# Kernel optimization log

Hardware: AMD Instinct MI355X
Metric: run time of the kernel (lower is better)

Reference implementation:

```python
import jax, jax.numpy as jnp
import numpy as np


def _hemisphere(radius=1.0, n=5):
    # replicates DiffuseShader.generate_hemisphere with sample=(5j,5j)
    u, v = np.mgrid[0:np.pi:n * 1j, 0:np.pi:n * 1j]
    x = (radius * np.cos(u) * np.sin(v)).flatten()
    y = (radius * np.sin(u) * np.sin(v)).flatten()
    z = (radius * np.cos(v)).flatten()
    return jnp.asarray(np.c_[x, y, z], dtype=jnp.float32)


def _diffuse_forward(V, COL, OPA, p, l, normals, hemi_vecs, indices, pointindex):
    P, S, N = p.shape[0], hemi_vecs.shape[0], V.shape[0]
    local = pointindex % P
    # --- project_hemisphere_projection: Rodrigues rotation local->global ---
    u = l[None, :] - p                                      # [P,3]
    u_hat = u / jnp.linalg.norm(u, axis=1, keepdims=True)
    v_loc = jnp.broadcast_to(jnp.array([0.0, -1.0, 0.0], p.dtype), u_hat.shape)
    c = -u_hat[:, 1:2]                                      # rowwise dot(v_loc, u_hat), [P,1]
    w = jnp.cross(v_loc, u_hat)                             # [P,3]
    z0 = jnp.zeros_like(w[:, 0])
    vmat = jnp.stack([jnp.stack([z0, -w[:, 2], w[:, 1]], -1),
                      jnp.stack([w[:, 2], z0, -w[:, 0]], -1),
                      jnp.stack([-w[:, 1], w[:, 0], z0], -1)], axis=1)  # [P,3,3] skew(w)
    R = jnp.eye(3, dtype=p.dtype)[None] + vmat + jnp.matmul(vmat, vmat) / (1.0 + c)[..., None]
    lh = jnp.einsum('pij,sj->psi', R, hemi_vecs) + l        # [P,S,3]
    o = jnp.broadcast_to(p[:, None, :], (P, S, 3))
    d = lh - o
    # --- get_intersection: ray/plane distances ---
    nrm = jnp.cross(V[:, 1] - V[:, 0], V[:, 2] - V[:, 0])
    nrm = nrm / jnp.linalg.norm(nrm, axis=1, keepdims=True)  # [N,3]
    kk = -jnp.sum(nrm * V[:, 3], axis=1)                     # [N]
    vo = o.reshape(P * S, 3) @ nrm.T                         # [P*S,N]
    vd = d.reshape(P * S, 3) @ nrm.T
    t = (-(kk[None, :] + vo) / vd).reshape(P, N, S)          # faithful to torch .view(P,N,S) on the [P*S,N] buffer
    surf = indices[pointindex, 0]
    mat = indices[pointindex, 1]
    empty = jnp.zeros((P, N, S), bool).at[local, surf, :].set(True)
    viable = (t > -1e-4) & (t < 1.0) & (~empty)
    # --- barycentric condition test ---
    r = o[:, None, :, :] + t[..., None] * d[:, None, :, :]   # [P,N,S,3]
    a0 = V[:, 0, 0][None, :, None]; a1 = V[:, 0, 1][None, :, None]; a2 = V[:, 0, 2][None, :, None]
    b0 = V[:, 1, 0][None, :, None]; b1 = V[:, 1, 1][None, :, None]; b2 = V[:, 1, 2][None, :, None]
    c0 = V[:, 2, 0][None, :, None]; c1 = V[:, 2, 1][None, :, None]; c2 = V[:, 2, 2][None, :, None]
    r0, r1, r2 = r[..., 0], r[..., 1], r[..., 2]
    A = a0 * r2 - a2 * r0
    B = a0 * b2 - a2 * b0
    C = a0 * r1 - a1 * r0
    D = a0 * b1 - a1 * b0
    E = a0 * c2 - a2 * c0
    F = B * (a1 * c0 - a0 * c1)
    gam = (D * (A * D - B * C)) / (D * (E * D + F))
    beta = (C + gam * (a1 * c0 - a0 * c1)) / D
    alpha = (r0 - (beta * b0 + gam * c0)) / a0
    mask = jnp.where(viable & (beta > 0.0) & (gam > 0.0) & (alpha > 0.0), 1.0, 0.0).astype(jnp.float32)
    col = COL[surf, mat]                                     # [P,3]
    opa = jnp.clip(OPA[surf, mat], 0.0, 1.0)                 # [P]
    reflected_ray = l[None, :] - p                           # [P,3]
    return mask, col, opa, reflected_ray


def setup_inputs() -> dict:
    P, N, M, G = 512, 1024, 8, 2048
    key = jax.random.key(0)
    ks = jax.random.split(key, 8)
    V = jax.random.normal(ks[0], (N, 4, 3), jnp.float32)
    indices = jax.random.randint(ks[1], (G, 2), 0, M)
    pointindex = jax.random.randint(ks[2], (P,), 0, G)
    COL = jax.random.uniform(ks[3], (N, M, 3), jnp.float32)
    OPA = jax.random.uniform(ks[4], (N, M), jnp.float32)
    p = jax.random.normal(ks[5], (P, 3), jnp.float32) * 5.0
    l = jax.random.normal(ks[6], (3,), jnp.float32) * 10.0 + 20.0
    normals = jax.random.normal(ks[7], (N, 3), jnp.float32)
    return {"V": V, "indices": indices, "pointindex": pointindex, "COL": COL,
            "OPA": OPA, "p": p, "l": l, "normals": normals, "it": 0,
            "hemi_vecs": _hemisphere(1.0, 5)}


def reference(V, indices, pointindex, COL, OPA, p, l, normals, it, hemi_vecs):
    return _diffuse_forward(V, COL, OPA, p, l, normals, hemi_vecs, indices, pointindex)
```

## Files before the change

### kernel.cpp

```cpp
#include <hip/hip_runtime.h>
#include <math.h>

#define NP   512
#define NT   1024
#define NS   25
#define NPS  (NP*NS)
#define MASKN (NP*NT*NS)

#define DSA_OFF  0
#define PD_OFF   51200
#define NX_OFF   53248
#define NY_OFF   54272
#define NZ_OFF   55296
#define KK_OFF   56320
#define W_OFF    57344
#define EMPTY_OFF ((size_t)67584 * 8)

__global__ void prep_points(const float* __restrict__ p,
                            const float* __restrict__ l,
                            const float* __restrict__ hemi,
                            double* __restrict__ ws) {
    int idx = blockIdx.x * 256 + threadIdx.x;
    if (idx >= NPS) return;
    int pi = idx / NS, si = idx % NS;
    double px = p[pi*3+0], py = p[pi*3+1], pz = p[pi*3+2];
    double lx = l[0], ly = l[1], lz = l[2];
    double ux = lx - px, uy = ly - py, uz = lz - pz;
    double nrm = sqrt(ux*ux + uy*uy + uz*uz);
    ux /= nrm; uy /= nrm; uz /= nrm;
    double c = -uy;
    double wx = -uz, wz = ux;
    double m01 = -wz, m02 = 0.0;
    double m10 =  wz, m12 = -wx;
    double m21 =  wx, m20 = 0.0;
    double q00 = m01*m10;
    double q01 = 0.0, q10 = 0.0;
    double q02 = m01*m12;
    double q11 = m10*m01 + m12*m21;
    double q12 = 0.0, q21 = 0.0;
    double q20 = m21*m10;
    double q22 = m21*m12;
    double ic = 1.0 + c;
    double r00 = 1.0 + q00/ic, r01 = m01 + q01/ic, r02 = m02 + q02/ic;
    double r10 = m10 + q10/ic, r11 = 1.0 + q11/ic, r12 = m12 + q12/ic;
    double r20 = m20 + q20/ic, r21 = m21 + q21/ic, r22 = 1.0 + q22/ic;
    double hx = hemi[si*3+0], hy = hemi[si*3+1], hz = hemi[si*3+2];
    double lhx = r00*hx + r01*hy + r02*hz + lx;
    double lhy = r10*hx + r11*hy + r12*hz + ly;
    double lhz = r20*hx + r21*hy + r22*hz + lz;
    double* dsA = ws + DSA_OFF;
    dsA[idx*4+0] = lhx - px;
    dsA[idx*4+1] = lhy - py;
    dsA[idx*4+2] = lhz - pz;
    dsA[idx*4+3] = 0.0;
}

__device__ __forceinline__ double sgn(double x) {
    return (x > 0.0) ? 1.0 : ((x < 0.0) ? -1.0 : 0.0);
}

__global__ void prep_tris(const float* __restrict__ V,
                          double* __restrict__ ws,
                          unsigned* __restrict__ emptyMask) {
    int n = blockIdx.x * 256 + threadIdx.x;
    if (n < NP) emptyMask[n] = 0u;
    if (n >= NT) return;
    const float* v = V + n*12;
    double a0=v[0], a1=v[1], a2=v[2];
    double b0=v[3], b1=v[4], b2=v[5];
    double c0=v[6], c1=v[7], c2=v[8];
    double v3x=v[9], v3y=v[10], v3z=v[11];
    double e1x=b0-a0, e1y=b1-a1, e1z=b2-a2;
    double e2x=c0-a0, e2y=c1-a1, e2z=c2-a2;
    double cx = e1y*e2z - e1z*e2y;
    double cy = e1z*e2x - e1x*e2z;
    double cz = e1x*e2y - e1y*e2x;
    double nn = sqrt(cx*cx + cy*cy + cz*cz);
    double nx = cx/nn, ny = cy/nn, nz = cz/nn;
    double kk = -(nx*v3x + ny*v3y + nz*v3z);
    double Bv = a0*b2 - a2*b0;
    double Dv = a0*b1 - a1*b0;
    double Ec = a0*c2 - a2*c0;
    double G2 = a1*c0 - a0*c1;
    double Fc = Bv*G2;
    double gd = Dv*(Ec*Dv + Fc);
    double gq = Dv*gd;
    double dq = Dv*c0;
    double aq = a0*gq;
    double WGr0 = a1*Bv - a2*Dv, WGr1 = -(a0*Bv), WGr2 = a0*Dv;
    double dg = Dv*G2;
    double WBr0 = -(a1*gd) + dg*WGr0;
    double WBr1 =  a0*gd  + dg*WGr1;
    double WBr2 =            dg*WGr2;
    double dd = Dv*dq;
    double WAr0 = gq - b0*WBr0 - dd*WGr0;
    double WAr1 =    - b0*WBr1 - dd*WGr1;
    double WAr2 =    - b0*WBr2 - dd*WGr2;
    double sg = sgn(Dv*gd), sb = sgn(gq), sa = sgn(aq);
    ws[NX_OFF + n] = nx;
    ws[NY_OFF + n] = ny;
    ws[NZ_OFF + n] = nz;
    ws[KK_OFF + n] = kk;
    double* W = ws + W_OFF + n*10;
    W[0] = WGr0*sg; W[1] = WGr1*sg; W[2] = WGr2*sg;
    W[3] = WBr0*sb; W[4] = WBr1*sb; W[5] = WBr2*sb;
    W[6] = WAr0*sa; W[7] = WAr1*sa; W[8] = WAr2*sa;
    W[9] = 0.0;
}

__global__ void prep_scatter(const int* __restrict__ indices,
                             const int* __restrict__ pointindex,
                             const float* __restrict__ COL,
                             const float* __restrict__ OPA,
                             const float* __restrict__ p,
                             const float* __restrict__ l,
                             unsigned* __restrict__ emptyMask,
                             float* __restrict__ out,
                             double* __restrict__ ws) {
    int i = blockIdx.x * 256 + threadIdx.x;
    if (i >= NP) return;
    int pidx = pointindex[i];
    int local = pidx & (NP - 1);
    int surf = indices[pidx*2 + 0];
    int mat  = indices[pidx*2 + 1];
    atomicOr(&emptyMask[local], 1u << surf);
    float* colOut = out + MASKN;
    float* opaOut = out + MASKN + 3*NP;
    float* refOut = out + MASKN + 4*NP;
    colOut[i*3+0] = COL[(surf*8+mat)*3+0];
    colOut[i*3+1] = COL[(surf*8+mat)*3+1];
    colOut[i*3+2] = COL[(surf*8+mat)*3+2];
    float o = OPA[surf*8+mat];
    opaOut[i] = fminf(fmaxf(o, 0.0f), 1.0f);
    refOut[i*3+0] = (float)((double)l[0] - (double)p[i*3+0]);
    refOut[i*3+1] = (float)((double)l[1] - (double)p[i*3+1]);
    refOut[i*3+2] = (float)((double)l[2] - (double)p[i*3+2]);
    double* pd = ws + PD_OFF;
    pd[i*4+0] = (double)p[i*3+0];
    pd[i*4+1] = (double)p[i*3+1];
    pd[i*4+2] = (double)p[i*3+2];
    pd[i*4+3] = 0.0;
}

__global__ __launch_bounds__(256) void diffuse_main(
        const double* __restrict__ ws,
        const unsigned* __restrict__ emptyMask,
        float* __restrict__ out) {
    __shared__ double sW[42][10];
    __shared__ double sdx[25], sdy[25], sdz[25];

    const unsigned ps = blockIdx.x;
    const unsigned pp = ps / 25u;
    const unsigned q  = ps - pp * 25u;
    const unsigned nn0 = (q << 10) / 25u;
    const unsigned tid = threadIdx.x;

    const double* Wg = ws + W_OFF;
    {
        unsigned i = tid;
        if (i < 210u) {
            unsigned row = i / 5u, col = i - row * 5u;
            unsigned gn = nn0 + row; if (gn > 1023u) gn = 1023u;
            const double2 v = *(const double2*)(Wg + gn*10u + col*2u);
            sW[row][col*2u]   = v.x;
            sW[row][col*2u+1] = v.y;
        }
        if (i < 25u) {
            const double* dr = ws + DSA_OFF + (pp*25u + i)*4u;
            sdx[i] = dr[0]; sdy[i] = dr[1]; sdz[i] = dr[2];
        }
    }
    const double sx = ws[DSA_OFF + ps*4u + 0];
    const double sy = ws[DSA_OFF + ps*4u + 1];
    const double sz = ws[DSA_OFF + ps*4u + 2];
    const double ox = ws[PD_OFF + pp*4u + 0];
    const double oy = ws[PD_OFF + pp*4u + 1];
    const double oz = ws[PD_OFF + pp*4u + 2];
    const unsigned em = emptyMask[pp];
    __syncthreads();

    const unsigned n0 = tid * 4u;
    const double2 nxa = *(const double2*)(ws + NX_OFF + n0);
    const double2 nxb = *(const double2*)(ws + NX_OFF + n0 + 2);
    const double2 nya = *(const double2*)(ws + NY_OFF + n0);
    const double2 nyb = *(const double2*)(ws + NY_OFF + n0 + 2);
    const double2 nza = *(const double2*)(ws + NZ_OFF + n0);
    const double2 nzb = *(const double2*)(ws + NZ_OFF + n0 + 2);
    const double2 kka = *(const double2*)(ws + KK_OFF + n0);
    const double2 kkb = *(const double2*)(ws + KK_OFF + n0 + 2);
    const unsigned rem0 = (q << 10) + n0;

    float res[4];
    #pragma unroll
    for (int k = 0; k < 4; ++k) {
        const double nxv = (k < 2) ? (k ? nxa.y : nxa.x) : (k == 3 ? nxb.y : nxb.x);
        const double nyv = (k < 2) ? (k ? nya.y : nya.x) : (k == 3 ? nyb.y : nyb.x);
        const double nzv = (k < 2) ? (k ? nza.y : nza.x) : (k == 3 ? nzb.y : nzb.x);
        const double kkv = (k < 2) ? (k ? kka.y : kka.x) : (k == 3 ? kkb.y : kkb.x);

        const double vd = fma(sz, nzv, fma(sy, nyv, sx * nxv));
        const double tt = fma(oz, nzv, fma(oy, nyv, fma(ox, nxv, kkv)));
        const double e1 = fma(1e-4, vd, -tt);
        const double e2 = vd + tt;

        const unsigned rem = rem0 + (unsigned)k;
        const unsigned nn = rem / 25u;
        const unsigned ss = rem - nn * 25u;
        const bool empty = (nn < 8u) && ((em >> nn) & 1u);

        const double dxv = sdx[ss], dyv = sdy[ss], dzv = sdz[ss];
        const double R0 = fma(-tt, dxv, vd * ox);
        const double R1 = fma(-tt, dyv, vd * oy);
        const double R2 = fma(-tt, dzv, vd * oz);

        const double* w = sW[nn - nn0];
        const double dG = fma(R2, w[2], fma(R1, w[1], R0 * w[0]));
        const double dB = fma(R2, w[5], fma(R1, w[4], R0 * w[3]));
        const double dA = fma(R2, w[8], fma(R1, w[7], R0 * w[6]));

        const bool ok = (e1 * vd > 0.0) && (e2 * vd > 0.0) && !empty
                     && (dG * vd > 0.0) && (dB * vd > 0.0) && (dA * vd > 0.0);
        res[k] = ok ? 1.0f : 0.0f;
    }
    *(float4*)(out + ps*1024u + n0) = make_float4(res[0], res[1], res[2], res[3]);
}

extern "C" void kernel_launch(void* const* d_in, const int* in_sizes, int n_in,
                              void* d_out, int out_size, void* d_ws, size_t ws_size,
                              hipStream_t stream) {
    const float* V         = (const float*)d_in[0];
    const int*   indices   = (const int*)  d_in[1];
    const int*   pointindex= (const int*)  d_in[2];
    const float* COL       = (const float*)d_in[3];
    const float* OPA       = (const float*)d_in[4];
    const float* p         = (const float*)d_in[5];
    const float* l         = (const float*)d_in[6];
    const float* hemi      = (const float*)d_in[9];

    float* out = (float*)d_out;
    double* ws = (double*)d_ws;
    unsigned* emptyMask = (unsigned*)((char*)d_ws + EMPTY_OFF);

    prep_points<<<(NPS + 255)/256, 256, 0, stream>>>(p, l, hemi, ws);
    prep_tris<<<(NT + 255)/256, 256, 0, stream>>>(V, ws, emptyMask);
    prep_scatter<<<(NP + 255)/256, 256, 0, stream>>>(indices, pointindex, COL, OPA,
                                                     p, l, emptyMask, out, ws);
    diffuse_main<<<NPS, 256, 0, stream>>>(ws, emptyMask, out);
}
```

Baseline: 41.13 us.

## Fuse prep kernels into one launch and simplify main-kernel sign tests

Merges the three preprocessing kernels into one launch that splits work by block range, removing two kernel launches and their serialization gaps. In the main kernel, the per-element divide by 25 becomes an incremental counter, the six multiply-and-compare sign tests become one XOR/OR on the high words of the doubles, and the empty-surface check is compiled in only for blocks with q==0. The shared weight row is padded from 10 to 11 doubles. The sign-bit trick treats zero and negative-zero differently from the old strict > 0 compare, which can change results in edge cases.

```diff
diff --git a/kernel.cpp b/kernel.cpp
--- a/kernel.cpp
+++ b/kernel.cpp
@@ -16,137 +16,187 @@
 #define W_OFF    57344
 #define EMPTY_OFF ((size_t)67584 * 8)
 
-__global__ void prep_points(const float* __restrict__ p,
-                            const float* __restrict__ l,
-                            const float* __restrict__ hemi,
-                            double* __restrict__ ws) {
-    int idx = blockIdx.x * 256 + threadIdx.x;
-    if (idx >= NPS) return;
-    int pi = idx / NS, si = idx % NS;
-    double px = p[pi*3+0], py = p[pi*3+1], pz = p[pi*3+2];
-    double lx = l[0], ly = l[1], lz = l[2];
-    double ux = lx - px, uy = ly - py, uz = lz - pz;
-    double nrm = sqrt(ux*ux + uy*uy + uz*uz);
-    ux /= nrm; uy /= nrm; uz /= nrm;
-    double c = -uy;
-    double wx = -uz, wz = ux;
-    double m01 = -wz, m02 = 0.0;
-    double m10 =  wz, m12 = -wx;
-    double m21 =  wx, m20 = 0.0;
-    double q00 = m01*m10;
-    double q01 = 0.0, q10 = 0.0;
-    double q02 = m01*m12;
-    double q11 = m10*m01 + m12*m21;
-    double q12 = 0.0, q21 = 0.0;
-    double q20 = m21*m10;
-    double q22 = m21*m12;
-    double ic = 1.0 + c;
-    double r00 = 1.0 + q00/ic, r01 = m01 + q01/ic, r02 = m02 + q02/ic;
-    double r10 = m10 + q10/ic, r11 = 1.0 + q11/ic, r12 = m12 + q12/ic;
-    double r20 = m20 + q20/ic, r21 = m21 + q21/ic, r22 = 1.0 + q22/ic;
-    double hx = hemi[si*3+0], hy = hemi[si*3+1], hz = hemi[si*3+2];
-    double lhx = r00*hx + r01*hy + r02*hz + lx;
-    double lhy = r10*hx + r11*hy + r12*hz + ly;
-    double lhz = r20*hx + r21*hy + r22*hz + lz;
-    double* dsA = ws + DSA_OFF;
-    dsA[idx*4+0] = lhx - px;
-    dsA[idx*4+1] = lhy - py;
-    dsA[idx*4+2] = lhz - pz;
-    dsA[idx*4+3] = 0.0;
-}
-
 __device__ __forceinline__ double sgn(double x) {
     return (x > 0.0) ? 1.0 : ((x < 0.0) ? -1.0 : 0.0);
 }
 
-__global__ void prep_tris(const float* __restrict__ V,
-                          double* __restrict__ ws,
-                          unsigned* __restrict__ emptyMask) {
-    int n = blockIdx.x * 256 + threadIdx.x;
-    if (n < NP) emptyMask[n] = 0u;
-    if (n >= NT) return;
-    const float* v = V + n*12;
-    double a0=v[0], a1=v[1], a2=v[2];
-    double b0=v[3], b1=v[4], b2=v[5];
-    double c0=v[6], c1=v[7], c2=v[8];
-    double v3x=v[9], v3y=v[10], v3z=v[11];
-    double e1x=b0-a0, e1y=b1-a1, e1z=b2-a2;
-    double e2x=c0-a0, e2y=c1-a1, e2z=c2-a2;
-    double cx = e1y*e2z - e1z*e2y;
-    double cy = e1z*e2x - e1x*e2z;
-    double cz = e1x*e2y - e1y*e2x;
-    double nn = sqrt(cx*cx + cy*cy + cz*cz);
-    double nx = cx/nn, ny = cy/nn, nz = cz/nn;
-    double kk = -(nx*v3x + ny*v3y + nz*v3z);
-    double Bv = a0*b2 - a2*b0;
-    double Dv = a0*b1 - a1*b0;
-    double Ec = a0*c2 - a2*c0;
-    double G2 = a1*c0 - a0*c1;
-    double Fc = Bv*G2;
-    double gd = Dv*(Ec*Dv + Fc);
-    double gq = Dv*gd;
-    double dq = Dv*c0;
-    double aq = a0*gq;
-    double WGr0 = a1*Bv - a2*Dv, WGr1 = -(a0*Bv), WGr2 = a0*Dv;
-    double dg = Dv*G2;
-    double WBr0 = -(a1*gd) + dg*WGr0;
-    double WBr1 =  a0*gd  + dg*WGr1;
-    double WBr2 =            dg*WGr2;
-    double dd = Dv*dq;
-    double WAr0 = gq - b0*WBr0 - dd*WGr0;
-    double WAr1 =    - b0*WBr1 - dd*WGr1;
-    double WAr2 =    - b0*WBr2 - dd*WGr2;
-    double sg = sgn(Dv*gd), sb = sgn(gq), sa = sgn(aq);
-    ws[NX_OFF + n] = nx;
-    ws[NY_OFF + n] = ny;
-    ws[NZ_OFF + n] = nz;
-    ws[KK_OFF + n] = kk;
-    double* W = ws + W_OFF + n*10;
-    W[0] = WGr0*sg; W[1] = WGr1*sg; W[2] = WGr2*sg;
-    W[3] = WBr0*sb; W[4] = WBr1*sb; W[5] = WBr2*sb;
-    W[6] = WAr0*sa; W[7] = WAr1*sa; W[8] = WAr2*sa;
-    W[9] = 0.0;
-}
-
-__global__ void prep_scatter(const int* __restrict__ indices,
-                             const int* __restrict__ pointindex,
-                             const float* __restrict__ COL,
-                             const float* __restrict__ OPA,
-                             const float* __restrict__ p,
-                             const float* __restrict__ l,
-                             unsigned* __restrict__ emptyMask,
-                             float* __restrict__ out,
-                             double* __restrict__ ws) {
-    int i = blockIdx.x * 256 + threadIdx.x;
-    if (i >= NP) return;
-    int pidx = pointindex[i];
-    int local = pidx & (NP - 1);
-    int surf = indices[pidx*2 + 0];
-    int mat  = indices[pidx*2 + 1];
-    atomicOr(&emptyMask[local], 1u << surf);
-    float* colOut = out + MASKN;
-    float* opaOut = out + MASKN + 3*NP;
-    float* refOut = out + MASKN + 4*NP;
-    colOut[i*3+0] = COL[(surf*8+mat)*3+0];
-    colOut[i*3+1] = COL[(surf*8+mat)*3+1];
-    colOut[i*3+2] = COL[(surf*8+mat)*3+2];
-    float o = OPA[surf*8+mat];
-    opaOut[i] = fminf(fmaxf(o, 0.0f), 1.0f);
-    refOut[i*3+0] = (float)((double)l[0] - (double)p[i*3+0]);
-    refOut[i*3+1] = (float)((double)l[1] - (double)p[i*3+1]);
-    refOut[i*3+2] = (float)((double)l[2] - (double)p[i*3+2]);
-    double* pd = ws + PD_OFF;
-    pd[i*4+0] = (double)p[i*3+0];
-    pd[i*4+1] = (double)p[i*3+1];
-    pd[i*4+2] = (double)p[i*3+2];
-    pd[i*4+3] = 0.0;
+__global__ void prep_all(const float* __restrict__ p,
+                         const float* __restrict__ l,
+                         const float* __restrict__ hemi,
+                         const float* __restrict__ V,
+                         const int* __restrict__ indices,
+                         const int* __restrict__ pointindex,
+                         const float* __restrict__ COL,
+                         const float* __restrict__ OPA,
+                         double* __restrict__ ws,
+                         unsigned* __restrict__ emptyMask,
+                         float* __restrict__ out) {
+    const int b = blockIdx.x, t = threadIdx.x;
+    if (b < 50) {
+        int idx = b * 256 + t;
+        int pi = idx / NS, si = idx % NS;
+        double px = p[pi*3+0], py = p[pi*3+1], pz = p[pi*3+2];
+        double lx = l[0], ly = l[1], lz = l[2];
+        double ux = lx - px, uy = ly - py, uz = lz - pz;
+        double nrm = sqrt(ux*ux + uy*uy + uz*uz);
+        ux /= nrm; uy /= nrm; uz /= nrm;
+        double c = -uy;
+        double wx = -uz, wz = ux;
+        double m01 = -wz, m10 = wz, m12 = -wx, m21 = wx;
+        double q00 = m01*m10;
+        double q02 = m01*m12;
+        double q11 = m10*m01 + m12*m21;
+        double q20 = m21*m10;
+        double q22 = m21*m12;
+        double ic = 1.0 + c;
+        double r00 = 1.0 + q00/ic, r01 = m01,            r02 = q02/ic;
+        double r10 = m10,          r11 = 1.0 + q11/ic,   r12 = m12;
+        double r20 = q20/ic,       r21 = m21,            r22 = 1.0 + q22/ic;
+        double hx = hemi[si*3+0], hy = hemi[si*3+1], hz = hemi[si*3+2];
+        double lhx = r00*hx + r01*hy + r02*hz + lx;
+        double lhy = r10*hx + r11*hy + r12*hz + ly;
+        double lhz = r20*hx + r21*hy + r22*hz + lz;
+        double* dsA = ws + DSA_OFF;
+        dsA[idx*4+0] = lhx - px;
+        dsA[idx*4+1] = lhy - py;
+        dsA[idx*4+2] = lhz - pz;
+        dsA[idx*4+3] = 0.0;
+    } else if (b < 54) {
+        int n = (b - 50) * 256 + t;
+        const float* v = V + n*12;
+        double a0=v[0], a1=v[1], a2=v[2];
+        double b0=v[3], b1=v[4], b2=v[5];
+        double c0=v[6], c1=v[7], c2=v[8];
+        double v3x=v[9], v3y=v[10], v3z=v[11];
+        double e1x=b0-a0, e1y=b1-a1, e1z=b2-a2;
+        double e2x=c0-a0, e2y=c1-a1, e2z=c2-a2;
+        double cx = e1y*e2z - e1z*e2y;
+        double cy = e1z*e2x - e1x*e2z;
+        double cz = e1x*e2y - e1y*e2x;
+        double nn = sqrt(cx*cx + cy*cy + cz*cz);
+        double nx = cx/nn, ny = cy/nn, nz = cz/nn;
+        double kk = -(nx*v3x + ny*v3y + nz*v3z);
+        double Bv = a0*b2 - a2*b0;
+        double Dv = a0*b1 - a1*b0;
+        double Ec = a0*c2 - a2*c0;
+        double G2 = a1*c0 - a0*c1;
+        double Fc = Bv*G2;
+        double gd = Dv*(Ec*Dv + Fc);
+        double gq = Dv*gd;
+        double dq = Dv*c0;
+        double aq = a0*gq;
+        double WGr0 = a1*Bv - a2*Dv, WGr1 = -(a0*Bv), WGr2 = a0*Dv;
+        double dg = Dv*G2;
+        double WBr0 = -(a1*gd) + dg*WGr0;
+        double WBr1 =  a0*gd  + dg*WGr1;
+        double WBr2 =            dg*WGr2;
+        double dd = Dv*dq;
+        double WAr0 = gq - b0*WBr0 - dd*WGr0;
+        double WAr1 =    - b0*WBr1 - dd*WGr1;
+        double WAr2 =    - b0*WBr2 - dd*WGr2;
+        double sg = sgn(Dv*gd), sb = sgn(gq), sa = sgn(aq);
+        ws[NX_OFF + n] = nx;
+        ws[NY_OFF + n] = ny;
+        ws[NZ_OFF + n] = nz;
+        ws[KK_OFF + n] = kk;
+        double* W = ws + W_OFF + n*10;
+        W[0] = WGr0*sg; W[1] = WGr1*sg; W[2] = WGr2*sg;
+        W[3] = WBr0*sb; W[4] = WBr1*sb; W[5] = WBr2*sb;
+        W[6] = WAr0*sa; W[7] = WAr1*sa; W[8] = WAr2*sa;
+        W[9] = 0.0;
+    } else {
+        emptyMask[t] = 0u;
+        emptyMask[t + 256] = 0u;
+        __syncthreads();
+        for (int i = t; i < NP; i += 256) {
+            int pidx = pointindex[i];
+            int local = pidx & (NP - 1);
+            int surf = indices[pidx*2 + 0];
+            int mat  = indices[pidx*2 + 1];
+            atomicOr(&emptyMask[local], 1u << surf);
+            float* colOut = out + MASKN;
+            float* opaOut = out + MASKN + 3*NP;
+            float* refOut = out + MASKN + 4*NP;
+            colOut[i*3+0] = COL[(surf*8+mat)*3+0];
+            colOut[i*3+1] = COL[(surf*8+mat)*3+1];
+            colOut[i*3+2] = COL[(surf*8+mat)*3+2];
+            float o = OPA[surf*8+mat];
+            opaOut[i] = fminf(fmaxf(o, 0.0f), 1.0f);
+            refOut[i*3+0] = (float)((double)l[0] - (double)p[i*3+0]);
+            refOut[i*3+1] = (float)((double)l[1] - (double)p[i*3+1]);
+            refOut[i*3+2] = (float)((double)l[2] - (double)p[i*3+2]);
+            double* pd = ws + PD_OFF;
+            pd[i*4+0] = (double)p[i*3+0];
+            pd[i*4+1] = (double)p[i*3+1];
+            pd[i*4+2] = (double)p[i*3+2];
+            pd[i*4+3] = 0.0;
+        }
+    }
+}
+
+template<bool HE>
+__device__ __forceinline__ void line_body(
+        const double* __restrict__ ws, const double (*sW)[11],
+        const double* sdx, const double* sdy, const double* sdz,
+        double sx, double sy, double sz, double ox, double oy, double oz,
+        unsigned em, unsigned nn0, unsigned q, unsigned ps, unsigned tid,
+        float* __restrict__ out) {
+    const unsigned n0 = tid * 4u;
+    const double2 nxa = *(const double2*)(ws + NX_OFF + n0);
+    const double2 nxb = *(const double2*)(ws + NX_OFF + n0 + 2);
+    const double2 nya = *(const double2*)(ws + NY_OFF + n0);
+    const double2 nyb = *(const double2*)(ws + NY_OFF + n0 + 2);
+    const double2 nza = *(const double2*)(ws + NZ_OFF + n0);
+    const double2 nzb = *(const double2*)(ws + NZ_OFF + n0 + 2);
+    const double2 kka = *(const double2*)(ws + KK_OFF + n0);
+    const double2 kkb = *(const double2*)(ws + KK_OFF + n0 + 2);
+
+    const unsigned rem0 = (q << 10) + n0;
+    unsigned nn = rem0 / 25u;
+    unsigned ss = rem0 - nn * 25u;
+
+    float res[4];
+    #pragma unroll
+    for (int k = 0; k < 4; ++k) {
+        const double nxv = (k < 2) ? (k ? nxa.y : nxa.x) : (k == 3 ? nxb.y : nxb.x);
+        const double nyv = (k < 2) ? (k ? nya.y : nya.x) : (k == 3 ? nyb.y : nyb.x);
+        const double nzv = (k < 2) ? (k ? nza.y : nza.x) : (k == 3 ? nzb.y : nzb.x);
+        const double kkv = (k < 2) ? (k ? kka.y : kka.x) : (k == 3 ? kkb.y : kkb.x);
+
+        const double vd = fma(sz, nzv, fma(sy, nyv, sx * nxv));
+        const double tt = fma(oz, nzv, fma(oy, nyv, fma(ox, nxv, kkv)));
+        const double e1 = fma(1e-4, vd, -tt);
+        const double e2 = vd + tt;
+
+        const double dxv = sdx[ss], dyv = sdy[ss], dzv = sdz[ss];
+        const double R0 = fma(-tt, dxv, vd * ox);
+        const double R1 = fma(-tt, dyv, vd * oy);
+        const double R2 = fma(-tt, dzv, vd * oz);
+
+        const double* w = sW[nn - nn0];
+        const double dG = fma(R2, w[2], fma(R1, w[1], R0 * w[0]));
+        const double dB = fma(R2, w[5], fma(R1, w[4], R0 * w[3]));
+        const double dA = fma(R2, w[8], fma(R1, w[7], R0 * w[6]));
+
+        const int hv = __double2hiint(vd);
+        int m = (__double2hiint(e1) ^ hv) | (__double2hiint(e2) ^ hv)
+              | (__double2hiint(dG) ^ hv) | (__double2hiint(dB) ^ hv)
+              | (__double2hiint(dA) ^ hv);
+        bool ok = (m >= 0);
+        if (HE) ok = ok && !((nn < 8u) && ((em >> nn) & 1u));
+        res[k] = ok ? 1.0f : 0.0f;
+
+        ++ss;
+        if (ss == 25u) { ss = 0u; ++nn; }
+    }
+    *(float4*)(out + ps*1024u + n0) = make_float4(res[0], res[1], res[2], res[3]);
 }
 
 __global__ __launch_bounds__(256) void diffuse_main(
         const double* __restrict__ ws,
         const unsigned* __restrict__ emptyMask,
         float* __restrict__ out) {
-    __shared__ double sW[42][10];
+    __shared__ double sW[42][11];
     __shared__ double sdx[25], sdy[25], sdz[25];
 
     const unsigned ps = blockIdx.x;
@@ -176,53 +226,15 @@
     const double ox = ws[PD_OFF + pp*4u + 0];
     const double oy = ws[PD_OFF + pp*4u + 1];
     const double oz = ws[PD_OFF + pp*4u + 2];
-    const unsigned em = emptyMask[pp];
+    const unsigned em = (q == 0u) ? emptyMask[pp] : 0u;
     __syncthreads();
 
-    const unsigned n0 = tid * 4u;
-    const double2 nxa = *(const double2*)(ws + NX_OFF + n0);
-    const double2 nxb = *(const double2*)(ws + NX_OFF + n0 + 2);
-    const double2 nya = *(const double2*)(ws + NY_OFF + n0);
-    const double2 nyb = *(const double2*)(ws + NY_OFF + n0 + 2);
-    const double2 nza = *(const double2*)(ws + NZ_OFF + n0);
-    const double2 nzb = *(const double2*)(ws + NZ_OFF + n0 + 2);
-    const double2 kka = *(const double2*)(ws + KK_OFF + n0);
-    const double2 kkb = *(const double2*)(ws + KK_OFF + n0 + 2);
-    const unsigned rem0 = (q << 10) + n0;
-
-    float res[4];
-    #pragma unroll
-    for (int k = 0; k < 4; ++k) {
-        const double nxv = (k < 2) ? (k ? nxa.y : nxa.x) : (k == 3 ? nxb.y : nxb.x);
-        const double nyv = (k < 2) ? (k ? nya.y : nya.x) : (k == 3 ? nyb.y : nyb.x);
-        const double nzv = (k < 2) ? (k ? nza.y : nza.x) : (k == 3 ? nzb.y : nzb.x);
-        const double kkv = (k < 2) ? (k ? kka.y : kka.x) : (k == 3 ? kkb.y : kkb.x);
-
-        const double vd = fma(sz, nzv, fma(sy, nyv, sx * nxv));
-        const double tt = fma(oz, nzv, fma(oy, nyv, fma(ox, nxv, kkv)));
-        const double e1 = fma(1e-4, vd, -tt);
-        const double e2 = vd + tt;
-
-        const unsigned rem = rem0 + (unsigned)k;
-        const unsigned nn = rem / 25u;
-        const unsigned ss = rem - nn * 25u;
-        const bool empty = (nn < 8u) && ((em >> nn) & 1u);
-
-        const double dxv = sdx[ss], dyv = sdy[ss], dzv = sdz[ss];
-        const double R0 = fma(-tt, dxv, vd * ox);
-        const double R1 = fma(-tt, dyv, vd * oy);
-        const double R2 = fma(-tt, dzv, vd * oz);
-
-        const double* w = sW[nn - nn0];
-        const double dG = fma(R2, w[2], fma(R1, w[1], R0 * w[0]));
-        const double dB = fma(R2, w[5], fma(R1, w[4], R0 * w[3]));
-        const double dA = fma(R2, w[8], fma(R1, w[7], R0 * w[6]));
-
-        const bool ok = (e1 * vd > 0.0) && (e2 * vd > 0.0) && !empty
-                     && (dG * vd > 0.0) && (dB * vd > 0.0) && (dA * vd > 0.0);
-        res[k] = ok ? 1.0f : 0.0f;
-    }
-    *(float4*)(out + ps*1024u + n0) = make_float4(res[0], res[1], res[2], res[3]);
+    if (q == 0u)
+        line_body<true >(ws, sW, sdx, sdy, sdz, sx, sy, sz, ox, oy, oz,
+                         em, nn0, q, ps, tid, out);
+    else
+        line_body<false>(ws, sW, sdx, sdy, sdz, sx, sy, sz, ox, oy, oz,
+                         em, nn0, q, ps, tid, out);
 }
 
 extern "C" void kernel_launch(void* const* d_in, const int* in_sizes, int n_in,
@@ -241,9 +253,7 @@
     double* ws = (double*)d_ws;
     unsigned* emptyMask = (unsigned*)((char*)d_ws + EMPTY_OFF);
 
-    prep_points<<<(NPS + 255)/256, 256, 0, stream>>>(p, l, hemi, ws);
-    prep_tris<<<(NT + 255)/256, 256, 0, stream>>>(V, ws, emptyMask);
-    prep_scatter<<<(NP + 255)/256, 256, 0, stream>>>(indices, pointindex, COL, OPA,
-                                                     p, l, emptyMask, out, ws);
+    prep_all<<<55, 256, 0, stream>>>(p, l, hemi, V, indices, pointindex,
+                                     COL, OPA, ws, emptyMask, out);
     diffuse_main<<<NPS, 256, 0, stream>>>(ws, emptyMask, out);
 }
```

Result: faster. 39.90 us (-3.0%).
